# Performance work log

Hardware: AMD Instinct MI355X
Metric: run time of the kernel (lower is better)

## Reference

```python
import jax, jax.numpy as jnp
import numpy as np
from jax import lax

RADIUS = (5, 5, 5)
EPS = 1e-5


def _box_sum(x, radius=RADIUS):
    # Separable all-ones box filter == F.conv3d(x, ones((1,1,)+radius), padding='same')
    # x: [N, 1, D, H, W]
    dn = lax.conv_dimension_numbers(x.shape, (1, 1) + radius, ('NCDHW', 'OIDHW', 'NCDHW'))
    for axis, k in zip((2, 3, 4), radius):
        kshape = [1, 1, 1, 1, 1]
        kshape[axis] = k
        kern = jnp.ones(kshape, dtype=x.dtype)
        dn_ax = lax.conv_dimension_numbers(x.shape, tuple(kshape), ('NCDHW', 'OIDHW', 'NCDHW'))
        x = lax.conv_general_dilated(x, kern, window_strides=(1, 1, 1), padding='SAME',
                                     dimension_numbers=dn_ax)
    return x


def _image_gradient(img):
    # torch.gradient over spatial dims (central diff interior, one-sided edges)
    g = jnp.gradient(img, axis=(2, 3, 4))
    return jnp.concatenate(g, axis=1)  # [N, 3, D, H, W]


def setup_inputs() -> dict:
    key = jax.random.key(0)
    k1, k2, k3, k4 = jax.random.split(key, 4)
    shape = (1, 1, 192, 192, 192)
    moving_image = jax.random.normal(k1, shape, dtype=jnp.float32)
    fixed_image = jax.random.normal(k2, shape, dtype=jnp.float32)
    moving_mask = jax.random.randint(k3, shape, 0, 2).astype(jnp.bool_)
    fixed_mask = jax.random.randint(k4, shape, 0, 2).astype(jnp.bool_)
    original_image_spacing = jnp.ones((3,), dtype=jnp.int32)
    return {
        'moving_image': moving_image,
        'fixed_image': fixed_image,
        'moving_mask': moving_mask,
        'fixed_mask': fixed_mask,
        'original_image_spacing': original_image_spacing,
    }


def reference(moving_image, fixed_image, moving_mask, fixed_mask, original_image_spacing):
    npix = float(np.prod(RADIUS))  # 125

    # dual method: union mask applied to both gradients, total grad halved
    union = jnp.logical_or(moving_mask, fixed_mask).astype(moving_image.dtype)
    grad_moving = _image_gradient(moving_image) * union
    grad_fixed = _image_gradient(fixed_image) * union
    total_grad = (grad_moving + grad_fixed) * 0.5

    sum_m = _box_sum(moving_image)
    sum_f = _box_sum(fixed_image)
    sum_mm = _box_sum(moving_image * moving_image)
    sum_ff = _box_sum(fixed_image * fixed_image)
    sum_mf = _box_sum(moving_image * fixed_image)

    moving_mean = sum_m / npix
    fixed_mean = sum_f / npix

    var_m = sum_mm - 2 * moving_mean * sum_m + npix * moving_mean * moving_mean
    var_f = sum_ff - 2 * fixed_mean * sum_f + npix * fixed_mean * fixed_mean
    var_mf = var_m * var_f
    cross = sum_mf - fixed_mean * sum_m - moving_mean * sum_f + npix * moving_mean * fixed_mean

    moving_mean_centered = moving_image - moving_mean
    fixed_mean_centered = fixed_image - fixed_mean

    mask = (var_mf > EPS) & (var_f > EPS) & (fixed_mean_centered != 0.0) & (moving_mean_centered != 0.0)
    var_mf_safe = jnp.where(mask, var_mf, 1.0)
    var_f_safe = jnp.where(mask, var_f, 1.0)
    factor = jnp.where(
        mask,
        2.0 * cross / var_mf_safe * (moving_mean_centered - cross * fixed_mean_centered / var_f_safe),
        0.0,
    )

    return -1.0 * factor * total_grad
```

## Files before the change

### kernel.cpp

```cpp
#include <hip/hip_runtime.h>


#define DD 192
#define HH 192
#define WW 192
#define NVOX (DD * HH * WW)
#define TS 16
#define RR 20
#define RW 24
#define ZSEG 12
#define NRING 5

__global__ __launch_bounds__(256)
void ncc_forces_kernel(const float* __restrict__ mimg,
                       const float* __restrict__ fimg,
                       const int*   __restrict__ mmask,
                       const int*   __restrict__ fmask,
                       float* __restrict__ out)
{
    __shared__ float rawm[NRING][RR][RW];
    __shared__ float rawf[NRING][RR][RW];
    __shared__ float xs[5][RR][TS];

    const int tx = threadIdx.x;
    const int ty = threadIdx.y;
    const int tid = ty * TS + tx;
    const int x0 = blockIdx.x * TS;
    const int y0 = blockIdx.y * TS;
    const int z0 = blockIdx.z * ZSEG;
    const int z1 = z0 + ZSEG;

    const int  simg   = tid / 120;
    const bool stager = (simg < 2);
    const int  st     = tid - simg * 120;
    const int  srow   = st / 6;
    const int  squad  = st - srow * 6;
    const int  sgy    = y0 - 2 + srow;
    const int  sgxb   = x0 - 4 + squad * 4;
    const bool rowin  = (sgy >= 0) && (sgy < HH);
    const bool fullx  = (sgxb >= 0) && (sgxb + 3 < WW);
    const float* simg_ptr = (simg == 1) ? fimg : mimg;
    float* slds_base = (simg == 1) ? &rawf[0][0][0] : &rawm[0][0][0];
    const int  sloff = srow * RW + squad * 4;

    auto prefetch = [&](int zc_, float4& p) {
        p.x = p.y = p.z = p.w = 0.f;
        if (stager && rowin && zc_ >= 0 && zc_ < DD) {
            const float* src = simg_ptr + ((size_t)zc_ * HH + sgy) * WW;
            if (fullx) {
                p = *(const float4*)(src + sgxb);
            } else {
                if (sgxb + 0 >= 0 && sgxb + 0 < WW) p.x = src[sgxb + 0];
                if (sgxb + 1 >= 0 && sgxb + 1 < WW) p.y = src[sgxb + 1];
                if (sgxb + 2 >= 0 && sgxb + 2 < WW) p.z = src[sgxb + 2];
                if (sgxb + 3 >= 0 && sgxb + 3 < WW) p.w = src[sgxb + 3];
            }
        }
    };

    float ring[5][5];
#pragma unroll
    for (int s = 0; s < 5; ++s)
#pragma unroll
        for (int f = 0; f < 5; ++f) ring[s][f] = 0.f;

    float4 pref;
    prefetch(z0 - 2, pref);

    for (int zc = z0 - 2; zc <= z1 + 1; ++zc) {
        const int sw = (zc + 10) % 5;

        if (stager) {
            *(float4*)(slds_base + sw * (RR * RW) + sloff) = pref;
        }
        prefetch(zc + 1, pref);

        const int z = zc - 2;
        const bool emitv = (z >= z0) && (z < z1);
        int um = 0, uf = 0;
        if (emitv) {
            const int vidx = (z * HH + (y0 + ty)) * WW + (x0 + tx);
            um = mmask[vidx];
            uf = fmask[vidx];
        }

        __syncthreads();

        for (int i = tid; i < RR * TS; i += 256) {
            const int y  = i >> 4;
            const int xo = i & 15;
            float sm = 0.f, sf = 0.f, smm = 0.f, sff = 0.f, smf = 0.f;
#pragma unroll
            for (int dx = 0; dx < 5; ++dx) {
                const float a = rawm[sw][y][xo + 2 + dx];
                const float b = rawf[sw][y][xo + 2 + dx];
                sm += a; sf += b; smm += a * a; sff += b * b; smf += a * b;
            }
            xs[0][y][xo] = sm;
            xs[1][y][xo] = sf;
            xs[2][y][xo] = smm;
            xs[3][y][xo] = sff;
            xs[4][y][xo] = smf;
        }

        __syncthreads();

        float s2d[5];
#pragma unroll
        for (int f = 0; f < 5; ++f) {
            float s = 0.f;
#pragma unroll
            for (int dy = 0; dy < 5; ++dy) s += xs[f][ty + dy][tx];
            s2d[f] = s;
        }
#pragma unroll
        for (int s = 0; s < 4; ++s)
#pragma unroll
            for (int f = 0; f < 5; ++f) ring[s][f] = ring[s + 1][f];
#pragma unroll
        for (int f = 0; f < 5; ++f) ring[4][f] = s2d[f];

        if (emitv) {
            float sum_m = 0.f, sum_f = 0.f, sum_mm = 0.f, sum_ff = 0.f, sum_mf = 0.f;
#pragma unroll
            for (int s = 0; s < 5; ++s) {
                sum_m  += ring[s][0];
                sum_f  += ring[s][1];
                sum_mm += ring[s][2];
                sum_ff += ring[s][3];
                sum_mf += ring[s][4];
            }
            const int gx = x0 + tx, gy = y0 + ty;
            const int sz  = (zc + 8) % 5;
            const int szm = (zc + 7) % 5;
            const int szp = (zc + 9) % 5;
            const int cy = ty + 2, cx = tx + 4;
            const float mc = rawm[sz][cy][cx];
            const float fc = rawf[sz][cy][cx];

            float gxm, gxf, gym, gyf, gzm, gzf;
            if (gx == 0)          { gxm = rawm[sz][cy][cx + 1] - mc;  gxf = rawf[sz][cy][cx + 1] - fc; }
            else if (gx == WW-1)  { gxm = mc - rawm[sz][cy][cx - 1];  gxf = fc - rawf[sz][cy][cx - 1]; }
            else {
                gxm = 0.5f * (rawm[sz][cy][cx + 1] - rawm[sz][cy][cx - 1]);
                gxf = 0.5f * (rawf[sz][cy][cx + 1] - rawf[sz][cy][cx - 1]);
            }
            if (gy == 0)          { gym = rawm[sz][cy + 1][cx] - mc;  gyf = rawf[sz][cy + 1][cx] - fc; }
            else if (gy == HH-1)  { gym = mc - rawm[sz][cy - 1][cx];  gyf = fc - rawf[sz][cy - 1][cx]; }
            else {
                gym = 0.5f * (rawm[sz][cy + 1][cx] - rawm[sz][cy - 1][cx]);
                gyf = 0.5f * (rawf[sz][cy + 1][cx] - rawf[sz][cy - 1][cx]);
            }
            if (z == 0)           { gzm = rawm[szp][cy][cx] - mc;     gzf = rawf[szp][cy][cx] - fc; }
            else if (z == DD-1)   { gzm = mc - rawm[szm][cy][cx];     gzf = fc - rawf[szm][cy][cx]; }
            else {
                gzm = 0.5f * (rawm[szp][cy][cx] - rawm[szm][cy][cx]);
                gzf = 0.5f * (rawf[szp][cy][cx] - rawf[szm][cy][cx]);
            }

            const float u = ((um != 0) || (uf != 0)) ? 1.0f : 0.0f;

            const float npix = 125.0f;
            const float inv_npix = 1.0f / 125.0f;
            const float mean_m = sum_m * inv_npix;
            const float mean_f = sum_f * inv_npix;
            const float var_m = sum_mm - 2.0f * mean_m * sum_m + npix * mean_m * mean_m;
            const float var_f = sum_ff - 2.0f * mean_f * sum_f + npix * mean_f * mean_f;
            const float var_mf = var_m * var_f;
            const float cross = sum_mf - mean_f * sum_m - mean_m * sum_f + npix * mean_m * mean_f;
            const float mmc = mc - mean_m;
            const float fmc = fc - mean_f;
            const bool ok = (var_mf > 1e-5f) && (var_f > 1e-5f) && (fmc != 0.0f) && (mmc != 0.0f);
            float factor = 0.0f;
            if (ok) factor = 2.0f * cross / var_mf * (mmc - cross * fmc / var_f);

            const int vidx = (z * HH + gy) * WW + gx;
            const float nf = -factor * 0.5f * u;
            out[vidx]            = nf * (gzm + gzf);
            out[NVOX + vidx]     = nf * (gym + gyf);
            out[2 * NVOX + vidx] = nf * (gxm + gxf);
        }
    }
}

extern "C" void kernel_launch(void* const* d_in, const int* in_sizes, int n_in,
                              void* d_out, int out_size, void* d_ws, size_t ws_size,
                              hipStream_t stream)
{
    const float* mimg  = (const float*)d_in[0];
    const float* fimg  = (const float*)d_in[1];
    const int*   mmask = (const int*)d_in[2];
    const int*   fmask = (const int*)d_in[3];
    float* out = (float*)d_out;

    dim3 grid(WW / TS, HH / TS, DD / ZSEG);
    dim3 block(TS, TS, 1);
    hipLaunchKernelGGL(ncc_forces_kernel, grid, block, 0, stream,
                       mimg, fimg, mmask, fmask, out);
}
```

Baseline: 230.0 us.

## Restructure box filter into sliding-window register passes with XCD-aware block remap

```diff
diff --git a/kernel.cpp b/kernel.cpp
--- a/kernel.cpp
+++ b/kernel.cpp
@@ -8,8 +8,11 @@
 #define TS 16
 #define RR 20
 #define RW 24
-#define ZSEG 12
-#define NRING 5
+#define ZSEG 16
+#define NBX 12
+#define NBY 12
+#define NBZ 12
+#define PER_XCD ((NBX * NBY * NBZ) / 8)
 
 __global__ __launch_bounds__(256)
 void ncc_forces_kernel(const float* __restrict__ mimg,
@@ -18,101 +21,158 @@
                        const int*   __restrict__ fmask,
                        float* __restrict__ out)
 {
-    __shared__ float rawm[NRING][RR][RW];
-    __shared__ float rawf[NRING][RR][RW];
-    __shared__ float xs[5][RR][TS];
-
-    const int tx = threadIdx.x;
-    const int ty = threadIdx.y;
-    const int tid = ty * TS + tx;
-    const int x0 = blockIdx.x * TS;
-    const int y0 = blockIdx.y * TS;
-    const int z0 = blockIdx.z * ZSEG;
-    const int z1 = z0 + ZSEG;
-
-    const int  simg   = tid / 120;
-    const bool stager = (simg < 2);
-    const int  st     = tid - simg * 120;
-    const int  srow   = st / 6;
-    const int  squad  = st - srow * 6;
-    const int  sgy    = y0 - 2 + srow;
-    const int  sgxb   = x0 - 4 + squad * 4;
-    const bool rowin  = (sgy >= 0) && (sgy < HH);
-    const bool fullx  = (sgxb >= 0) && (sgxb + 3 < WW);
-    const float* simg_ptr = (simg == 1) ? fimg : mimg;
-    float* slds_base = (simg == 1) ? &rawf[0][0][0] : &rawm[0][0][0];
-    const int  sloff = srow * RW + squad * 4;
-
-    auto prefetch = [&](int zc_, float4& p) {
-        p.x = p.y = p.z = p.w = 0.f;
-        if (stager && rowin && zc_ >= 0 && zc_ < DD) {
-            const float* src = simg_ptr + ((size_t)zc_ * HH + sgy) * WW;
-            if (fullx) {
-                p = *(const float4*)(src + sgxb);
-            } else {
-                if (sgxb + 0 >= 0 && sgxb + 0 < WW) p.x = src[sgxb + 0];
-                if (sgxb + 1 >= 0 && sgxb + 1 < WW) p.y = src[sgxb + 1];
-                if (sgxb + 2 >= 0 && sgxb + 2 < WW) p.z = src[sgxb + 2];
-                if (sgxb + 3 >= 0 && sgxb + 3 < WW) p.w = src[sgxb + 3];
+    __shared__ float rawm[4][RR][RW];
+    __shared__ float rawf[4][RR][RW];
+    __shared__ float xs[5][RR][20];
+    __shared__ float box[5][TS][17];
+
+    const int b  = blockIdx.x;
+    const int L  = (b & 7) * PER_XCD + (b >> 3);
+    const int bz = L / (NBX * NBY);
+    const int r0_ = L - bz * (NBX * NBY);
+    const int by = r0_ / NBX;
+    const int bx = r0_ - by * NBX;
+
+    const int tid = threadIdx.x;
+    const int tx = tid & 15;
+    const int ty = tid >> 4;
+    const int x0 = bx * TS, y0 = by * TS, z0 = bz * ZSEG;
+
+    const bool is_xs = (tid < 80);
+    const int  xrow  = tid >> 2;
+    const int  xj    = tid & 3;
+    const int  xgy   = y0 - 2 + xrow;
+    const int  gx0   = x0 + 4 * xj;
+    const bool xrowin = (xgy >= 0) && (xgy < HH);
+    const bool lok    = (gx0 > 0);
+    const bool rok    = (gx0 + 4 < WW);
+
+    const int  t2   = tid - 80;
+    const bool is_raw = (tid >= 80) && (tid < 200);
+    const int  rrow = t2 / 6;
+    const int  rq   = t2 - rrow * 6;
+    const int  rgy  = y0 - 2 + rrow;
+    const int  rgx  = x0 - 4 + 4 * rq;
+    const bool rrowin = (rgy >= 0) && (rgy < HH);
+    const bool rxin   = (rgx >= 0) && (rgx <= WW - 4);
+
+    float4 qm = make_float4(0,0,0,0), qf = qm, prm_ = qm, prf_ = qm;
+    float2 lm = make_float2(0,0), lf = lm, rm2 = lm, rf2 = lm;
+
+    auto prefetch = [&](int zz) {
+        if (is_xs) {
+            qm = qf = make_float4(0,0,0,0);
+            lm = lf = rm2 = rf2 = make_float2(0,0);
+            if (zz >= 0 && zz < DD && xrowin) {
+                const float* pm = mimg + ((size_t)zz * HH + xgy) * WW;
+                const float* pf = fimg + ((size_t)zz * HH + xgy) * WW;
+                qm = *(const float4*)(pm + gx0);
+                qf = *(const float4*)(pf + gx0);
+                if (lok) { lm  = *(const float2*)(pm + gx0 - 2); lf  = *(const float2*)(pf + gx0 - 2); }
+                if (rok) { rm2 = *(const float2*)(pm + gx0 + 4); rf2 = *(const float2*)(pf + gx0 + 4); }
+            }
+        } else if (is_raw) {
+            prm_ = prf_ = make_float4(0,0,0,0);
+            if (zz >= 0 && zz < DD && rrowin && rxin) {
+                prm_ = *(const float4*)(mimg + ((size_t)zz * HH + rgy) * WW + rgx);
+                prf_ = *(const float4*)(fimg + ((size_t)zz * HH + rgy) * WW + rgx);
             }
         }
     };
 
+    auto commit = [&](int slot) {
+        if (is_xs) {
+            float a[8]  = {lm.x, lm.y, qm.x, qm.y, qm.z, qm.w, rm2.x, rm2.y};
+            float bb[8] = {lf.x, lf.y, qf.x, qf.y, qf.z, qf.w, rf2.x, rf2.y};
+            float s, w0, w1, w2, w3;
+            s = a[0]+a[1]+a[2]+a[3]+a[4]; w0=s; s+=a[5]-a[0]; w1=s; s+=a[6]-a[1]; w2=s; s+=a[7]-a[2]; w3=s;
+            *(float4*)&xs[0][xrow][4*xj] = make_float4(w0,w1,w2,w3);
+            s = bb[0]+bb[1]+bb[2]+bb[3]+bb[4]; w0=s; s+=bb[5]-bb[0]; w1=s; s+=bb[6]-bb[1]; w2=s; s+=bb[7]-bb[2]; w3=s;
+            *(float4*)&xs[1][xrow][4*xj] = make_float4(w0,w1,w2,w3);
+            {
+                float p[8];
+#pragma unroll
+                for (int i = 0; i < 8; ++i) p[i] = a[i]*a[i];
+                s = p[0]+p[1]+p[2]+p[3]+p[4]; w0=s; s+=p[5]-p[0]; w1=s; s+=p[6]-p[1]; w2=s; s+=p[7]-p[2]; w3=s;
+                *(float4*)&xs[2][xrow][4*xj] = make_float4(w0,w1,w2,w3);
+            }
+            {
+                float p[8];
+#pragma unroll
+                for (int i = 0; i < 8; ++i) p[i] = bb[i]*bb[i];
+                s = p[0]+p[1]+p[2]+p[3]+p[4]; w0=s; s+=p[5]-p[0]; w1=s; s+=p[6]-p[1]; w2=s; s+=p[7]-p[2]; w3=s;
+                *(float4*)&xs[3][xrow][4*xj] = make_float4(w0,w1,w2,w3);
+            }
+            {
+                float p[8];
+#pragma unroll
+                for (int i = 0; i < 8; ++i) p[i] = a[i]*bb[i];
+                s = p[0]+p[1]+p[2]+p[3]+p[4]; w0=s; s+=p[5]-p[0]; w1=s; s+=p[6]-p[1]; w2=s; s+=p[7]-p[2]; w3=s;
+                *(float4*)&xs[4][xrow][4*xj] = make_float4(w0,w1,w2,w3);
+            }
+        } else if (is_raw) {
+            *(float4*)&rawm[slot][rrow][4*rq] = prm_;
+            *(float4*)&rawf[slot][rrow][4*rq] = prf_;
+        }
+    };
+
+    auto ytask = [&](int t) {
+        const int x = t & 15;
+        const int c = (t >> 4) & 3;
+        const int f = t >> 6;
+        const float* col = &xs[f][4*c][x];
+        const float v0 = col[0],   v1 = col[20],  v2 = col[40],  v3 = col[60];
+        const float v4 = col[80],  v5 = col[100], v6 = col[120], v7 = col[140];
+        float s = v0 + v1 + v2 + v3 + v4;
+        float* bp = &box[f][x][4*c];
+        bp[0] = s; s += v5 - v0;
+        bp[1] = s; s += v6 - v1;
+        bp[2] = s; s += v7 - v2;
+        bp[3] = s;
+    };
+
     float ring[5][5];
 #pragma unroll
     for (int s = 0; s < 5; ++s)
 #pragma unroll
         for (int f = 0; f < 5; ++f) ring[s][f] = 0.f;
-
-    float4 pref;
-    prefetch(z0 - 2, pref);
-
-    for (int zc = z0 - 2; zc <= z1 + 1; ++zc) {
-        const int sw = (zc + 10) % 5;
-
-        if (stager) {
-            *(float4*)(slds_base + sw * (RR * RW) + sloff) = pref;
-        }
-        prefetch(zc + 1, pref);
-
-        const int z = zc - 2;
-        const bool emitv = (z >= z0) && (z < z1);
+    float cm0=0, cm1=0, cm2=0, cm3=0, cf0=0, cf1=0, cf2=0, cf3=0;
+
+    prefetch(z0 - 2);
+
+    for (int n = 0; n < ZSEG + 4; ++n) {
+        const int zc   = z0 - 2 + n;
+        const int slot = n & 3;
+
+        commit(slot);
+        prefetch(zc + 1);
+
+        const int  z = zc - 2;
+        const bool emitv = (n >= 4);
         int um = 0, uf = 0;
         if (emitv) {
             const int vidx = (z * HH + (y0 + ty)) * WW + (x0 + tx);
-            um = mmask[vidx];
-            uf = fmask[vidx];
+            um = __builtin_nontemporal_load(mmask + vidx);
+            uf = __builtin_nontemporal_load(fmask + vidx);
         }
 
         __syncthreads();
 
-        for (int i = tid; i < RR * TS; i += 256) {
-            const int y  = i >> 4;
-            const int xo = i & 15;
-            float sm = 0.f, sf = 0.f, smm = 0.f, sff = 0.f, smf = 0.f;
-#pragma unroll
-            for (int dx = 0; dx < 5; ++dx) {
-                const float a = rawm[sw][y][xo + 2 + dx];
-                const float b = rawf[sw][y][xo + 2 + dx];
-                sm += a; sf += b; smm += a * a; sff += b * b; smf += a * b;
-            }
-            xs[0][y][xo] = sm;
-            xs[1][y][xo] = sf;
-            xs[2][y][xo] = smm;
-            xs[3][y][xo] = sff;
-            xs[4][y][xo] = smf;
-        }
+        ytask(tid);
+        if (tid < 64) ytask(tid + 256);
 
         __syncthreads();
 
+        {
+            const float ncm = rawm[slot][ty + 2][tx + 4];
+            const float ncf = rawf[slot][ty + 2][tx + 4];
+            cm3 = cm2; cm2 = cm1; cm1 = cm0; cm0 = ncm;
+            cf3 = cf2; cf2 = cf1; cf1 = cf0; cf0 = ncf;
+        }
+
         float s2d[5];
 #pragma unroll
-        for (int f = 0; f < 5; ++f) {
-            float s = 0.f;
-#pragma unroll
-            for (int dy = 0; dy < 5; ++dy) s += xs[f][ty + dy][tx];
-            s2d[f] = s;
-        }
+        for (int f = 0; f < 5; ++f) s2d[f] = box[f][tx][ty];
 #pragma unroll
         for (int s = 0; s < 4; ++s)
 #pragma unroll
@@ -131,32 +191,27 @@
                 sum_mf += ring[s][4];
             }
             const int gx = x0 + tx, gy = y0 + ty;
-            const int sz  = (zc + 8) % 5;
-            const int szm = (zc + 7) % 5;
-            const int szp = (zc + 9) % 5;
+            const int slot2 = (n + 2) & 3;
             const int cy = ty + 2, cx = tx + 4;
-            const float mc = rawm[sz][cy][cx];
-            const float fc = rawf[sz][cy][cx];
+            const float mc = cm2;
+            const float fc = cf2;
 
             float gxm, gxf, gym, gyf, gzm, gzf;
-            if (gx == 0)          { gxm = rawm[sz][cy][cx + 1] - mc;  gxf = rawf[sz][cy][cx + 1] - fc; }
-            else if (gx == WW-1)  { gxm = mc - rawm[sz][cy][cx - 1];  gxf = fc - rawf[sz][cy][cx - 1]; }
+            if (gx == 0)          { gxm = rawm[slot2][cy][cx + 1] - mc;  gxf = rawf[slot2][cy][cx + 1] - fc; }
+            else if (gx == WW-1)  { gxm = mc - rawm[slot2][cy][cx - 1];  gxf = fc - rawf[slot2][cy][cx - 1]; }
             else {
-                gxm = 0.5f * (rawm[sz][cy][cx + 1] - rawm[sz][cy][cx - 1]);
-                gxf = 0.5f * (rawf[sz][cy][cx + 1] - rawf[sz][cy][cx - 1]);
-            }
-            if (gy == 0)          { gym = rawm[sz][cy + 1][cx] - mc;  gyf = rawf[sz][cy + 1][cx] - fc; }
-            else if (gy == HH-1)  { gym = mc - rawm[sz][cy - 1][cx];  gyf = fc - rawf[sz][cy - 1][cx]; }
+                gxm = 0.5f * (rawm[slot2][cy][cx + 1] - rawm[slot2][cy][cx - 1]);
+                gxf = 0.5f * (rawf[slot2][cy][cx + 1] - rawf[slot2][cy][cx - 1]);
+            }
+            if (gy == 0)          { gym = rawm[slot2][cy + 1][cx] - mc;  gyf = rawf[slot2][cy + 1][cx] - fc; }
+            else if (gy == HH-1)  { gym = mc - rawm[slot2][cy - 1][cx];  gyf = fc - rawf[slot2][cy - 1][cx]; }
             else {
-                gym = 0.5f * (rawm[sz][cy + 1][cx] - rawm[sz][cy - 1][cx]);
-                gyf = 0.5f * (rawf[sz][cy + 1][cx] - rawf[sz][cy - 1][cx]);
-            }
-            if (z == 0)           { gzm = rawm[szp][cy][cx] - mc;     gzf = rawf[szp][cy][cx] - fc; }
-            else if (z == DD-1)   { gzm = mc - rawm[szm][cy][cx];     gzf = fc - rawf[szm][cy][cx]; }
-            else {
-                gzm = 0.5f * (rawm[szp][cy][cx] - rawm[szm][cy][cx]);
-                gzf = 0.5f * (rawf[szp][cy][cx] - rawf[szm][cy][cx]);
-            }
+                gym = 0.5f * (rawm[slot2][cy + 1][cx] - rawm[slot2][cy - 1][cx]);
+                gyf = 0.5f * (rawf[slot2][cy + 1][cx] - rawf[slot2][cy - 1][cx]);
+            }
+            if (z == 0)           { gzm = cm1 - mc;            gzf = cf1 - fc; }
+            else if (z == DD-1)   { gzm = mc - cm3;            gzf = fc - cf3; }
+            else                  { gzm = 0.5f * (cm1 - cm3);  gzf = 0.5f * (cf1 - cf3); }
 
             const float u = ((um != 0) || (uf != 0)) ? 1.0f : 0.0f;
 
@@ -193,8 +248,8 @@
     const int*   fmask = (const int*)d_in[3];
     float* out = (float*)d_out;
 
-    dim3 grid(WW / TS, HH / TS, DD / ZSEG);
-    dim3 block(TS, TS, 1);
+    dim3 grid(NBX * NBY * NBZ, 1, 1);
+    dim3 block(256, 1, 1);
     hipLaunchKernelGGL(ncc_forces_kernel, grid, block, 0, stream,
                        mimg, fimg, mmask, fmask, out);
 }
```

Result: slower. 247.6 us (+7.6%).

## Pipeline y-pass box sums one z-step ahead and remap blocks across XCDs

Applied to the files above, without the earlier changes.

```diff
diff --git a/kernel.cpp b/kernel.cpp
--- a/kernel.cpp
+++ b/kernel.cpp
@@ -9,7 +9,10 @@
 #define RR 20
 #define RW 24
 #define ZSEG 12
-#define NRING 5
+#define NBX 12
+#define NBY 12
+#define NBZ 16
+#define PER_XCD ((NBX * NBY * NBZ) / 8)
 
 __global__ __launch_bounds__(256)
 void ncc_forces_kernel(const float* __restrict__ mimg,
@@ -18,17 +21,21 @@
                        const int*   __restrict__ fmask,
                        float* __restrict__ out)
 {
-    __shared__ float rawm[NRING][RR][RW];
-    __shared__ float rawf[NRING][RR][RW];
-    __shared__ float xs[5][RR][TS];
-
-    const int tx = threadIdx.x;
-    const int ty = threadIdx.y;
-    const int tid = ty * TS + tx;
-    const int x0 = blockIdx.x * TS;
-    const int y0 = blockIdx.y * TS;
-    const int z0 = blockIdx.z * ZSEG;
-    const int z1 = z0 + ZSEG;
+    __shared__ float rawm[5][RR][RW];
+    __shared__ float rawf[5][RR][RW];
+    __shared__ float xs[5][RR][20];
+    __shared__ float box[2][5][TS][20];
+
+    const int b  = blockIdx.x;
+    const int L  = (b & 7) * PER_XCD + (b >> 3);
+    const int bz = L / (NBX * NBY);
+    const int r_ = L - bz * (NBX * NBY);
+    const int by = r_ / NBX;
+    const int bx = r_ - by * NBX;
+
+    const int tid = threadIdx.x;
+    const int tx = tid & 15, ty = tid >> 4;
+    const int x0 = bx * TS, y0 = by * TS, z0 = bz * ZSEG;
 
     const int  simg   = tid / 120;
     const bool stager = (simg < 2);
@@ -36,26 +43,17 @@
     const int  srow   = st / 6;
     const int  squad  = st - srow * 6;
     const int  sgy    = y0 - 2 + srow;
-    const int  sgxb   = x0 - 4 + squad * 4;
-    const bool rowin  = (sgy >= 0) && (sgy < HH);
-    const bool fullx  = (sgxb >= 0) && (sgxb + 3 < WW);
-    const float* simg_ptr = (simg == 1) ? fimg : mimg;
-    float* slds_base = (simg == 1) ? &rawf[0][0][0] : &rawm[0][0][0];
-    const int  sloff = srow * RW + squad * 4;
-
-    auto prefetch = [&](int zc_, float4& p) {
-        p.x = p.y = p.z = p.w = 0.f;
-        if (stager && rowin && zc_ >= 0 && zc_ < DD) {
-            const float* src = simg_ptr + ((size_t)zc_ * HH + sgy) * WW;
-            if (fullx) {
-                p = *(const float4*)(src + sgxb);
-            } else {
-                if (sgxb + 0 >= 0 && sgxb + 0 < WW) p.x = src[sgxb + 0];
-                if (sgxb + 1 >= 0 && sgxb + 1 < WW) p.y = src[sgxb + 1];
-                if (sgxb + 2 >= 0 && sgxb + 2 < WW) p.z = src[sgxb + 2];
-                if (sgxb + 3 >= 0 && sgxb + 3 < WW) p.w = src[sgxb + 3];
-            }
-        }
+    const int  sgx    = x0 - 4 + 4 * squad;
+    const bool sin_   = (sgy >= 0) && (sgy < HH) && (sgx >= 0) && (sgx <= WW - 4);
+    const float* sptr = (simg == 1) ? fimg : mimg;
+    float* sldsb = (simg == 1) ? &rawf[0][0][0] : &rawm[0][0][0];
+    const int  sloff  = srow * RW + 4 * squad;
+
+    float4 pref = make_float4(0, 0, 0, 0);
+    auto prefetch = [&](int zz) {
+        pref = make_float4(0, 0, 0, 0);
+        if (stager && sin_ && zz >= 0 && zz < DD)
+            pref = *(const float4*)(sptr + ((size_t)zz * HH + sgy) * WW + sgx);
     };
 
     float ring[5][5];
@@ -63,62 +61,75 @@
     for (int s = 0; s < 5; ++s)
 #pragma unroll
         for (int f = 0; f < 5; ++f) ring[s][f] = 0.f;
-
-    float4 pref;
-    prefetch(z0 - 2, pref);
-
-    for (int zc = z0 - 2; zc <= z1 + 1; ++zc) {
-        const int sw = (zc + 10) % 5;
-
-        if (stager) {
-            *(float4*)(slds_base + sw * (RR * RW) + sloff) = pref;
-        }
-        prefetch(zc + 1, pref);
-
-        const int z = zc - 2;
-        const bool emitv = (z >= z0) && (z < z1);
+    float cm[5] = {0, 0, 0, 0, 0}, cf[5] = {0, 0, 0, 0, 0};
+
+    prefetch(z0 - 2);
+
+    for (int n = 0; n <= ZSEG + 4; ++n) {
+        const int zc = z0 - 2 + n;
+        const int sw = n % 5;
+        const int z  = zc - 3;
+        const bool emitv = (n >= 5);
+
+        if (stager) *(float4*)(sldsb + sw * (RR * RW) + sloff) = pref;
+        prefetch(zc + 1);
+
         int um = 0, uf = 0;
+        int vidx = 0;
         if (emitv) {
-            const int vidx = (z * HH + (y0 + ty)) * WW + (x0 + tx);
-            um = mmask[vidx];
-            uf = fmask[vidx];
+            vidx = (z * HH + (y0 + ty)) * WW + (x0 + tx);
+            um = __builtin_nontemporal_load(mmask + vidx);
+            uf = __builtin_nontemporal_load(fmask + vidx);
         }
 
         __syncthreads();
 
-        for (int i = tid; i < RR * TS; i += 256) {
-            const int y  = i >> 4;
-            const int xo = i & 15;
-            float sm = 0.f, sf = 0.f, smm = 0.f, sff = 0.f, smf = 0.f;
-#pragma unroll
-            for (int dx = 0; dx < 5; ++dx) {
-                const float a = rawm[sw][y][xo + 2 + dx];
-                const float b = rawf[sw][y][xo + 2 + dx];
-                sm += a; sf += b; smm += a * a; sff += b * b; smf += a * b;
-            }
-            xs[0][y][xo] = sm;
-            xs[1][y][xo] = sf;
-            xs[2][y][xo] = smm;
-            xs[3][y][xo] = sff;
-            xs[4][y][xo] = smf;
-        }
-
-        __syncthreads();
-
-        float s2d[5];
-#pragma unroll
-        for (int f = 0; f < 5; ++f) {
-            float s = 0.f;
-#pragma unroll
-            for (int dy = 0; dy < 5; ++dy) s += xs[f][ty + dy][tx];
-            s2d[f] = s;
-        }
-#pragma unroll
-        for (int s = 0; s < 4; ++s)
-#pragma unroll
-            for (int f = 0; f < 5; ++f) ring[s][f] = ring[s + 1][f];
-#pragma unroll
-        for (int f = 0; f < 5; ++f) ring[4][f] = s2d[f];
+        if (tid < 80) {
+            const int yy = tid >> 2;
+            const int t4 = (tid & 3) * 4;
+            const float4 A0 = *(const float4*)&rawm[sw][yy][t4];
+            const float4 A1 = *(const float4*)&rawm[sw][yy][t4 + 4];
+            const float2 A2 = *(const float2*)&rawm[sw][yy][t4 + 8];
+            const float4 B0 = *(const float4*)&rawf[sw][yy][t4];
+            const float4 B1 = *(const float4*)&rawf[sw][yy][t4 + 4];
+            const float2 B2 = *(const float2*)&rawf[sw][yy][t4 + 8];
+            const float a[10] = {A0.x, A0.y, A0.z, A0.w, A1.x, A1.y, A1.z, A1.w, A2.x, A2.y};
+            const float bb[10] = {B0.x, B0.y, B0.z, B0.w, B1.x, B1.y, B1.z, B1.w, B2.x, B2.y};
+            float p[10], s, w0, w1, w2, w3;
+#pragma unroll
+            for (int f = 0; f < 5; ++f) {
+#pragma unroll
+                for (int i = 2; i < 10; ++i) {
+                    p[i] = (f == 0) ? a[i] : (f == 1) ? bb[i] :
+                           (f == 2) ? a[i] * a[i] : (f == 3) ? bb[i] * bb[i] : a[i] * bb[i];
+                }
+                s = p[2] + p[3] + p[4] + p[5] + p[6]; w0 = s;
+                s += p[7] - p[2]; w1 = s;
+                s += p[8] - p[3]; w2 = s;
+                s += p[9] - p[4]; w3 = s;
+                *(float4*)&xs[f][yy][t4] = make_float4(w0, w1, w2, w3);
+            }
+        }
+
+        {
+            const float ncm = rawm[sw][ty + 2][tx + 4];
+            const float ncf = rawf[sw][ty + 2][tx + 4];
+#pragma unroll
+            for (int s2 = 4; s2 > 0; --s2) { cm[s2] = cm[s2 - 1]; cf[s2] = cf[s2 - 1]; }
+            cm[0] = ncm; cf[0] = ncf;
+        }
+        if (n >= 1) {
+            const int pp = (n - 1) & 1;
+            float s2d[5];
+#pragma unroll
+            for (int f = 0; f < 5; ++f) s2d[f] = box[pp][f][tx][ty];
+#pragma unroll
+            for (int s = 0; s < 4; ++s)
+#pragma unroll
+                for (int f = 0; f < 5; ++f) ring[s][f] = ring[s + 1][f];
+#pragma unroll
+            for (int f = 0; f < 5; ++f) ring[4][f] = s2d[f];
+        }
 
         if (emitv) {
             float sum_m = 0.f, sum_f = 0.f, sum_mm = 0.f, sum_ff = 0.f, sum_mf = 0.f;
@@ -131,32 +142,27 @@
                 sum_mf += ring[s][4];
             }
             const int gx = x0 + tx, gy = y0 + ty;
-            const int sz  = (zc + 8) % 5;
-            const int szm = (zc + 7) % 5;
-            const int szp = (zc + 9) % 5;
+            const int s2 = (n + 2) % 5;
             const int cy = ty + 2, cx = tx + 4;
-            const float mc = rawm[sz][cy][cx];
-            const float fc = rawf[sz][cy][cx];
+            const float mc = cm[3];
+            const float fc = cf[3];
 
             float gxm, gxf, gym, gyf, gzm, gzf;
-            if (gx == 0)          { gxm = rawm[sz][cy][cx + 1] - mc;  gxf = rawf[sz][cy][cx + 1] - fc; }
-            else if (gx == WW-1)  { gxm = mc - rawm[sz][cy][cx - 1];  gxf = fc - rawf[sz][cy][cx - 1]; }
+            if (gx == 0)          { gxm = rawm[s2][cy][cx + 1] - mc;  gxf = rawf[s2][cy][cx + 1] - fc; }
+            else if (gx == WW-1)  { gxm = mc - rawm[s2][cy][cx - 1];  gxf = fc - rawf[s2][cy][cx - 1]; }
             else {
-                gxm = 0.5f * (rawm[sz][cy][cx + 1] - rawm[sz][cy][cx - 1]);
-                gxf = 0.5f * (rawf[sz][cy][cx + 1] - rawf[sz][cy][cx - 1]);
-            }
-            if (gy == 0)          { gym = rawm[sz][cy + 1][cx] - mc;  gyf = rawf[sz][cy + 1][cx] - fc; }
-            else if (gy == HH-1)  { gym = mc - rawm[sz][cy - 1][cx];  gyf = fc - rawf[sz][cy - 1][cx]; }
+                gxm = 0.5f * (rawm[s2][cy][cx + 1] - rawm[s2][cy][cx - 1]);
+                gxf = 0.5f * (rawf[s2][cy][cx + 1] - rawf[s2][cy][cx - 1]);
+            }
+            if (gy == 0)          { gym = rawm[s2][cy + 1][cx] - mc;  gyf = rawf[s2][cy + 1][cx] - fc; }
+            else if (gy == HH-1)  { gym = mc - rawm[s2][cy - 1][cx];  gyf = fc - rawf[s2][cy - 1][cx]; }
             else {
-                gym = 0.5f * (rawm[sz][cy + 1][cx] - rawm[sz][cy - 1][cx]);
-                gyf = 0.5f * (rawf[sz][cy + 1][cx] - rawf[sz][cy - 1][cx]);
-            }
-            if (z == 0)           { gzm = rawm[szp][cy][cx] - mc;     gzf = rawf[szp][cy][cx] - fc; }
-            else if (z == DD-1)   { gzm = mc - rawm[szm][cy][cx];     gzf = fc - rawf[szm][cy][cx]; }
-            else {
-                gzm = 0.5f * (rawm[szp][cy][cx] - rawm[szm][cy][cx]);
-                gzf = 0.5f * (rawf[szp][cy][cx] - rawf[szm][cy][cx]);
-            }
+                gym = 0.5f * (rawm[s2][cy + 1][cx] - rawm[s2][cy - 1][cx]);
+                gyf = 0.5f * (rawf[s2][cy + 1][cx] - rawf[s2][cy - 1][cx]);
+            }
+            if (z == 0)           { gzm = cm[2] - mc;             gzf = cf[2] - fc; }
+            else if (z == DD-1)   { gzm = mc - cm[4];             gzf = fc - cf[4]; }
+            else                  { gzm = 0.5f * (cm[2] - cm[4]); gzf = 0.5f * (cf[2] - cf[4]); }
 
             const float u = ((um != 0) || (uf != 0)) ? 1.0f : 0.0f;
 
@@ -174,11 +180,29 @@
             float factor = 0.0f;
             if (ok) factor = 2.0f * cross / var_mf * (mmc - cross * fmc / var_f);
 
-            const int vidx = (z * HH + gy) * WW + gx;
             const float nf = -factor * 0.5f * u;
             out[vidx]            = nf * (gzm + gzf);
             out[NVOX + vidx]     = nf * (gym + gyf);
             out[2 * NVOX + vidx] = nf * (gxm + gxf);
+        }
+
+        __syncthreads();
+
+        if (tid < 160) {
+            const int x  = tid & 15;
+            const int c8 = ((tid >> 4) & 1) * 8;
+            const int f  = tid >> 5;
+            float v[12];
+#pragma unroll
+            for (int j = 0; j < 12; ++j) v[j] = xs[f][c8 + j][x];
+            float o[8];
+            float s = v[0] + v[1] + v[2] + v[3] + v[4];
+            o[0] = s;
+#pragma unroll
+            for (int j = 1; j < 8; ++j) { s += v[j + 4] - v[j - 1]; o[j] = s; }
+            float* bp = &box[n & 1][f][x][c8];
+            *(float4*)bp       = make_float4(o[0], o[1], o[2], o[3]);
+            *(float4*)(bp + 4) = make_float4(o[4], o[5], o[6], o[7]);
         }
     }
 }
@@ -193,8 +217,8 @@
     const int*   fmask = (const int*)d_in[3];
     float* out = (float*)d_out;
 
-    dim3 grid(WW / TS, HH / TS, DD / ZSEG);
-    dim3 block(TS, TS, 1);
+    dim3 grid(NBX * NBY * NBZ, 1, 1);
+    dim3 block(256, 1, 1);
     hipLaunchKernelGGL(ncc_forces_kernel, grid, block, 0, stream,
                        mimg, fimg, mmask, fmask, out);
 }
```

After: 213.8 us. 7.0% less time.
